# Kernel optimization log

Hardware: AMD Instinct MI355X
Metric: run time of the kernel (lower is better)

Reference implementation:

```python
import jax, jax.numpy as jnp
import numpy as np

D = 1024

def setup_inputs() -> dict:
    key = jax.random.key(0)
    kx, kw = jax.random.split(key)
    x = jax.random.normal(kx, (4, 2048, D), dtype=jnp.float32)
    # nn.Linear(d, 3d, bias=False): weight [3d, d]; y = x @ W.T
    W = jax.random.normal(kw, (3 * D, D), dtype=jnp.float32) * (1.0 / np.sqrt(D))
    return {"x": x, "W": W}

def reference(x, W):
    d = x.shape[-1]
    qkv = jnp.einsum('bsd,ed->bse', x, W)  # [B,S,3d]
    q, k, v = jnp.split(qkv, 3, axis=2)
    att = jnp.einsum('bqd,bkd->bqk', q, k) * (1.0 / jnp.sqrt(jnp.asarray(d, x.dtype)))
    att = jax.nn.softmax(att, axis=-1)
    y = jnp.einsum('bqk,bkd->bqd', att, v)
    return y
```

## Files before the change

### kernel.cpp

```cpp
#include <hip/hip_runtime.h>
#include <hip/hip_bf16.h>

typedef __attribute__((ext_vector_type(8))) short short8;
typedef __attribute__((ext_vector_type(4))) float f32x4;

typedef unsigned short u16;

__device__ __forceinline__ u16 f32_to_bf16(float f) {
    unsigned int u = __float_as_uint(f);
    u += 0x7fffu + ((u >> 16) & 1u);
    return (u16)(u >> 16);
}

__device__ __forceinline__ void gload16(const u16* g, u16* lds_base) {
    __builtin_amdgcn_global_load_lds(
        (const __attribute__((address_space(1))) void*)g,
        (__attribute__((address_space(3))) void*)lds_base, 16, 0, 0);
}

__device__ __forceinline__ void bar() { __builtin_amdgcn_s_barrier(); }
__device__ __forceinline__ void bar_end() {
    __builtin_amdgcn_sched_barrier(0);
    __builtin_amdgcn_s_barrier();
}
__device__ __forceinline__ void wait_vm8() {
    asm volatile("s_waitcnt vmcnt(8)" ::: "memory");
}
__device__ __forceinline__ void wait_vm7() {
    asm volatile("s_waitcnt vmcnt(7)" ::: "memory");
}
__device__ __forceinline__ void wait_vm6() {
    asm volatile("s_waitcnt vmcnt(6)" ::: "memory");
}
__device__ __forceinline__ void wait_vm0() {
    asm volatile("s_waitcnt vmcnt(0)" ::: "memory");
}

__global__ void cast_inputs(const float* __restrict__ x, u16* __restrict__ Xb,
                            const float* __restrict__ W, u16* __restrict__ Wb,
                            float* __restrict__ l,
                            int nx4, int nw4, int nl) {
    int i = blockIdx.x * blockDim.x + threadIdx.x;
    if (i >= nx4 + nw4) {
        int idx = i - (nx4 + nw4);
        if (idx < nl) l[idx] = 0.f;
        return;
    }
    const float* in; u16* out; int idx;
    if (i < nx4) { in = x; out = Xb; idx = i; }
    else { idx = i - nx4; in = W; out = Wb; }
    float4 v = ((const float4*)in)[idx];
    ushort4 o;
    o.x = f32_to_bf16(v.x); o.y = f32_to_bf16(v.y);
    o.z = f32_to_bf16(v.z); o.w = f32_to_bf16(v.w);
    ((ushort4*)out)[idx] = o;
}


struct Acc256 { f32x4 acc[8][4]; };
struct Acc192 { f32x4 acc[8][3]; };
struct Acc128 { f32x4 acc[8][2]; };

template<int MH>
__device__ __forceinline__ void rd_a(const u16* __restrict__ sA, int wr, int lane,
                                     int lr, short8 (&af)[4][2]) {
#pragma unroll
    for (int a2 = 0; a2 < 4; ++a2) {
        const int row = wr * 128 + MH * 64 + a2 * 16 + lr;
#pragma unroll
        for (int k2 = 0; k2 < 2; ++k2) {
            const int cb = (lane >> 4) + k2 * 4;
            af[a2][k2] = *(const short8*)(sA + row * 64 + ((cb ^ (lr & 7)) * 8));
        }
    }
}

template<int NH>
__device__ __forceinline__ void rd_b(const u16* __restrict__ sB, int wc, int lane,
                                     int lr, short8 (&bf)[2][2]) {
#pragma unroll
    for (int b2 = 0; b2 < 2; ++b2) {
        const int row = wc * 64 + NH * 32 + b2 * 16 + lr;
#pragma unroll
        for (int k2 = 0; k2 < 2; ++k2) {
            const int cb = (lane >> 4) + k2 * 4;
            bf[b2][k2] = *(const short8*)(sB + row * 64 + ((cb ^ (lr & 7)) * 8));
        }
    }
}

template<int MH, int NH>
__device__ __forceinline__ void mm_q(Acc256& fr, const short8 (&af)[4][2],
                                     const short8 (&bf)[2][2]) {
    __builtin_amdgcn_s_setprio(1);
#pragma unroll
    for (int a2 = 0; a2 < 4; ++a2)
#pragma unroll
        for (int b2 = 0; b2 < 2; ++b2)
#pragma unroll
            for (int k2 = 0; k2 < 2; ++k2)
                fr.acc[MH * 4 + a2][NH * 2 + b2] =
                    __builtin_amdgcn_mfma_f32_16x16x32_bf16(
                        af[a2][k2], bf[b2][k2],
                        fr.acc[MH * 4 + a2][NH * 2 + b2], 0, 0, 0);
    __builtin_amdgcn_s_setprio(0);
}

__device__ __forceinline__ void rd_b01(const u16* __restrict__ sB, int wc, int lane,
                                       int lr, short8 (&bf)[2][2]) {
#pragma unroll
    for (int b2 = 0; b2 < 2; ++b2) {
        const int row = wc * 48 + b2 * 16 + lr;
#pragma unroll
        for (int k2 = 0; k2 < 2; ++k2) {
            const int cb = (lane >> 4) + k2 * 4;
            bf[b2][k2] = *(const short8*)(sB + row * 64 + ((cb ^ (lr & 7)) * 8));
        }
    }
}

__device__ __forceinline__ void rd_b2(const u16* __restrict__ sB, int wc, int lane,
                                      int lr, short8 (&bf)[2]) {
    const int row = wc * 48 + 32 + lr;
#pragma unroll
    for (int k2 = 0; k2 < 2; ++k2) {
        const int cb = (lane >> 4) + k2 * 4;
        bf[k2] = *(const short8*)(sB + row * 64 + ((cb ^ (lr & 7)) * 8));
    }
}

template<int MH>
__device__ __forceinline__ void mm_b01(Acc192& fr, const short8 (&af)[4][2],
                                       const short8 (&bf)[2][2]) {
    __builtin_amdgcn_s_setprio(1);
#pragma unroll
    for (int a2 = 0; a2 < 4; ++a2)
#pragma unroll
        for (int b2 = 0; b2 < 2; ++b2)
#pragma unroll
            for (int k2 = 0; k2 < 2; ++k2)
                fr.acc[MH * 4 + a2][b2] =
                    __builtin_amdgcn_mfma_f32_16x16x32_bf16(
                        af[a2][k2], bf[b2][k2],
                        fr.acc[MH * 4 + a2][b2], 0, 0, 0);
    __builtin_amdgcn_s_setprio(0);
}

template<int MH>
__device__ __forceinline__ void mm_b2(Acc192& fr, const short8 (&af)[4][2],
                                      const short8 (&bf)[2]) {
    __builtin_amdgcn_s_setprio(1);
#pragma unroll
    for (int a2 = 0; a2 < 4; ++a2)
#pragma unroll
        for (int k2 = 0; k2 < 2; ++k2)
            fr.acc[MH * 4 + a2][2] =
                __builtin_amdgcn_mfma_f32_16x16x32_bf16(
                    af[a2][k2], bf[k2], fr.acc[MH * 4 + a2][2], 0, 0, 0);
    __builtin_amdgcn_s_setprio(0);
}

__device__ __forceinline__ void rd_bb(const u16* __restrict__ sB, int wc, int lane,
                                      int lr, short8 (&bf)[2][2]) {
#pragma unroll
    for (int b2 = 0; b2 < 2; ++b2) {
        const int row = wc * 32 + b2 * 16 + lr;
#pragma unroll
        for (int k2 = 0; k2 < 2; ++k2) {
            const int cb = (lane >> 4) + k2 * 4;
            bf[b2][k2] = *(const short8*)(sB + row * 64 + ((cb ^ (lr & 7)) * 8));
        }
    }
}

template<int MH>
__device__ __forceinline__ void mm_n128(Acc128& fr, const short8 (&af)[4][2],
                                        const short8 (&bf)[2][2]) {
    __builtin_amdgcn_s_setprio(1);
#pragma unroll
    for (int a2 = 0; a2 < 4; ++a2)
#pragma unroll
        for (int b2 = 0; b2 < 2; ++b2)
#pragma unroll
            for (int k2 = 0; k2 < 2; ++k2)
                fr.acc[MH * 4 + a2][b2] =
                    __builtin_amdgcn_mfma_f32_16x16x32_bf16(
                        af[a2][k2], bf[b2][k2],
                        fr.acc[MH * 4 + a2][b2], 0, 0, 0);
    __builtin_amdgcn_s_setprio(0);
}

__device__ __forceinline__ void gemm_core_256(
    const u16* __restrict__ A, const u16* __restrict__ Bt,
    int K, int lda, int ldb, int row0, int col0, u16* sm, Acc256& fr)
{
    const int t    = threadIdx.x;
    const int lane = t & 63;
    const int wave = t >> 6;
    const int wr   = wave >> 2;
    const int wc   = wave & 3;
    const int lr   = lane & 15;
    const int srow = lane >> 3;
    const int gc   = (lane & 7) ^ srow;

    const u16* const sA0 = sm;
    const u16* const sA1 = sm + 16384;
    const u16* const sB0 = sm + 32768;
    const u16* const sB1 = sm + 49152;

#pragma unroll
    for (int a = 0; a < 8; ++a)
#pragma unroll
        for (int b = 0; b < 4; ++b)
            fr.acc[a][b] = (f32x4){0.f, 0.f, 0.f, 0.f};

    const u16* aB = A  + (long long)(row0 + wave * 8 + srow) * lda + gc * 8;
    const u16* bB = Bt + (long long)(col0 + wave * 8 + srow) * ldb + gc * 8;
    u16* const sAw = sm + wave * 512;
    u16* const sBw = sm + 32768 + wave * 512;

    auto stageA = [&](int kt) {
        u16* d = sAw + (kt & 1) * 16384;
        const u16* g = aB + kt * 64;
#pragma unroll
        for (int r4 = 0; r4 < 4; ++r4)
            gload16(g + (long long)(r4 * 64) * lda, d + r4 * 4096);
    };
    auto stageB = [&](int kt) {
        u16* d = sBw + (kt & 1) * 16384;
        const u16* g = bB + kt * 64;
#pragma unroll
        for (int r4 = 0; r4 < 4; ++r4)
            gload16(g + (long long)(r4 * 64) * ldb, d + r4 * 4096);
    };

    stageA(0); stageB(0); stageA(1); stageB(1);
    wait_vm8();
    bar();

    const int NI = K >> 7;
    short8 af[4][2], bfa[2][2], bfb[2][2];
#pragma unroll 1
    for (int i = 0; i < NI; ++i) {
        const bool more = (i + 1 < NI);
        const int t2 = 2 * i + 2;

        rd_a<0>(sA0, wr, lane, lr, af);
        rd_b<0>(sB0, wc, lane, lr, bfa);
        bar();
        mm_q<0, 0>(fr, af, bfa);
        bar_end();

        rd_b<1>(sB0, wc, lane, lr, bfb);
        bar();
        mm_q<0, 1>(fr, af, bfb);
        bar_end();

        rd_a<1>(sA0, wr, lane, lr, af);
        if (more) stageB(t2);
        bar();
        mm_q<1, 1>(fr, af, bfb);
        bar_end();

        if (more) stageA(t2);
        bar();
        mm_q<1, 0>(fr, af, bfa);
        if (more) wait_vm8(); else wait_vm0();
        bar_end();

        rd_a<0>(sA1, wr, lane, lr, af);
        rd_b<0>(sB1, wc, lane, lr, bfa);
        bar();
        mm_q<0, 0>(fr, af, bfa);
        bar_end();

        rd_b<1>(sB1, wc, lane, lr, bfb);
        bar();
        mm_q<0, 1>(fr, af, bfb);
        bar_end();

        rd_a<1>(sA1, wr, lane, lr, af);
        if (more) stageB(t2 + 1);
        bar();
        mm_q<1, 1>(fr, af, bfb);
        bar_end();

        if (more) stageA(t2 + 1);
        bar();
        mm_q<1, 0>(fr, af, bfa);
        if (more) wait_vm8();
        bar_end();
    }
}

__device__ __forceinline__ void gemm_core_192(
    const u16* __restrict__ A, const u16* __restrict__ Bt,
    int K, int lda, int ldb, int row0, int col0, u16* sm, Acc192& fr)
{
    const int t    = threadIdx.x;
    const int lane = t & 63;
    const int wave = t >> 6;
    const int wr   = wave >> 2;
    const int wc   = wave & 3;
    const int lr   = lane & 15;
    const int srow = lane >> 3;
    const int gc   = (lane & 7) ^ srow;

    const u16* const sA0 = sm;
    const u16* const sA1 = sm + 16384;
    const u16* const sB0 = sm + 32768;
    const u16* const sB1 = sm + 45056;

#pragma unroll
    for (int a = 0; a < 8; ++a)
#pragma unroll
        for (int b = 0; b < 3; ++b)
            fr.acc[a][b] = (f32x4){0.f, 0.f, 0.f, 0.f};

    const u16* aB = A  + (long long)(row0 + wave * 8 + srow) * lda + gc * 8;
    const u16* bB = Bt + (long long)(col0 + wave * 8 + srow) * ldb + gc * 8;
    u16* const sAw = sm + wave * 512;
    u16* const sBw = sm + 32768 + wave * 512;

    auto stageA = [&](int kt) {
        u16* d = sAw + (kt & 1) * 16384;
        const u16* g = aB + kt * 64;
#pragma unroll
        for (int r4 = 0; r4 < 4; ++r4)
            gload16(g + (long long)(r4 * 64) * lda, d + r4 * 4096);
    };
    auto stageB = [&](int kt) {
        u16* d = sBw + (kt & 1) * 12288;
        const u16* g = bB + kt * 64;
#pragma unroll
        for (int r4 = 0; r4 < 3; ++r4)
            gload16(g + (long long)(r4 * 64) * ldb, d + r4 * 4096);
    };

    stageA(0); stageB(0); stageA(1); stageB(1);
    wait_vm7();
    bar();

    const int NI = K >> 7;
    short8 af[4][2], bfa[2][2], bfb[2];
#pragma unroll 1
    for (int i = 0; i < NI; ++i) {
        const bool more = (i + 1 < NI);
        const int t2 = 2 * i + 2;

        rd_a<0>(sA0, wr, lane, lr, af);
        rd_b01(sB0, wc, lane, lr, bfa);
        bar();
        mm_b01<0>(fr, af, bfa);
        bar_end();

        rd_b2(sB0, wc, lane, lr, bfb);
        bar();
        mm_b2<0>(fr, af, bfb);
        bar_end();

        rd_a<1>(sA0, wr, lane, lr, af);
        if (more) stageB(t2);
        bar();
        mm_b2<1>(fr, af, bfb);
        bar_end();

        if (more) stageA(t2);
        bar();
        mm_b01<1>(fr, af, bfa);
        if (more) wait_vm7(); else wait_vm0();
        bar_end();

        rd_a<0>(sA1, wr, lane, lr, af);
        rd_b01(sB1, wc, lane, lr, bfa);
        bar();
        mm_b01<0>(fr, af, bfa);
        bar_end();

        rd_b2(sB1, wc, lane, lr, bfb);
        bar();
        mm_b2<0>(fr, af, bfb);
        bar_end();

        rd_a<1>(sA1, wr, lane, lr, af);
        if (more) stageB(t2 + 1);
        bar();
        mm_b2<1>(fr, af, bfb);
        bar_end();

        if (more) stageA(t2 + 1);
        bar();
        mm_b01<1>(fr, af, bfa);
        if (more) wait_vm7();
        bar_end();
    }
}

__device__ __forceinline__ void gemm_core_n128(
    const u16* __restrict__ A, const u16* __restrict__ Bt,
    int K, int lda, int ldb, int row0, int col0, u16* sm, Acc128& fr)
{
    const int t    = threadIdx.x;
    const int lane = t & 63;
    const int wave = t >> 6;
    const int wr   = wave >> 2;
    const int wc   = wave & 3;
    const int lr   = lane & 15;
    const int srow = lane >> 3;
    const int gc   = (lane & 7) ^ srow;

    const u16* const sA0 = sm;
    const u16* const sA1 = sm + 16384;
    const u16* const sB0 = sm + 32768;
    const u16* const sB1 = sm + 40960;

#pragma unroll
    for (int a = 0; a < 8; ++a)
#pragma unroll
        for (int b = 0; b < 2; ++b)
            fr.acc[a][b] = (f32x4){0.f, 0.f, 0.f, 0.f};

    const u16* aB = A  + (long long)(row0 + wave * 8 + srow) * lda + gc * 8;
    const u16* bB = Bt + (long long)(col0 + wave * 8 + srow) * ldb + gc * 8;
    u16* const sAw = sm + wave * 512;
    u16* const sBw = sm + 32768 + wave * 512;

    auto stageA = [&](int kt) {
        u16* d = sAw + (kt & 1) * 16384;
        const u16* g = aB + kt * 64;
#pragma unroll
        for (int r4 = 0; r4 < 4; ++r4)
            gload16(g + (long long)(r4 * 64) * lda, d + r4 * 4096);
    };
    auto stageB = [&](int kt) {
        u16* d = sBw + (kt & 1) * 8192;
        const u16* g = bB + kt * 64;
#pragma unroll
        for (int r4 = 0; r4 < 2; ++r4)
            gload16(g + (long long)(r4 * 64) * ldb, d + r4 * 4096);
    };

    stageB(0); stageA(0); stageB(1); stageA(1);
    wait_vm6();
    bar();

    const int NI = K >> 7;
    short8 af[4][2], bf[2][2];
#pragma unroll 1
    for (int i = 0; i < NI; ++i) {
        const bool more = (i + 1 < NI);
        const int t2 = 2 * i + 2;

        rd_a<0>(sA0, wr, lane, lr, af);
        rd_bb(sB0, wc, lane, lr, bf);
        if (more) stageB(t2);
        bar();
        mm_n128<0>(fr, af, bf);
        bar_end();

        rd_a<1>(sA0, wr, lane, lr, af);
        if (more) stageA(t2);
        bar();
        mm_n128<1>(fr, af, bf);
        if (more) wait_vm6(); else wait_vm0();
        bar_end();

        rd_a<0>(sA1, wr, lane, lr, af);
        rd_bb(sB1, wc, lane, lr, bf);
        if (more) stageB(t2 + 1);
        bar();
        mm_n128<0>(fr, af, bf);
        bar_end();

        rd_a<1>(sA1, wr, lane, lr, af);
        if (more) stageA(t2 + 1);
        bar();
        mm_n128<1>(fr, af, bf);
        if (more) wait_vm6();
        bar_end();
    }
}


__global__ __launch_bounds__(512, 1) void gemm_qkv(
    const u16* __restrict__ Xb, const u16* __restrict__ Wb,
    u16* __restrict__ QK, u16* __restrict__ VT)
{
    __shared__ u16 sm[57344];
    const int row0 = blockIdx.y * 256;
    const int col0 = blockIdx.x * 192;

    Acc192 fr;
    gemm_core_192(Xb, Wb, 1024, 1024, 1024, row0, col0, sm, fr);

    const int lane = threadIdx.x & 63;
    const int wave = threadIdx.x >> 6;
    const int wr = wave >> 2, wc = wave & 3;
    const int cr = (lane >> 4) * 4, cc = lane & 15;

#pragma unroll
    for (int a = 0; a < 8; ++a) {
        const int grow = row0 + wr * 128 + a * 16 + cr;
#pragma unroll
        for (int b = 0; b < 3; ++b) {
            const int gcol = col0 + wc * 48 + b * 16 + cc;
            if (gcol < 2048) {
#pragma unroll
                for (int r = 0; r < 4; ++r)
                    QK[(long long)(grow + r) * 2048 + gcol] =
                        f32_to_bf16(fr.acc[a][b][r]);
            } else {
                const int bz = grow >> 11, s = grow & 2047;
                const int d = gcol - 2048;
                ushort4 o;
                o.x = f32_to_bf16(fr.acc[a][b][0]);
                o.y = f32_to_bf16(fr.acc[a][b][1]);
                o.z = f32_to_bf16(fr.acc[a][b][2]);
                o.w = f32_to_bf16(fr.acc[a][b][3]);
                *(ushort4*)(&VT[((long long)(bz * 1024 + d)) * 2048 + s]) = o;
            }
        }
    }
}

__global__ __launch_bounds__(512, 1) void gemm_s_exp(
    const u16* __restrict__ QK, u16* __restrict__ E, float* __restrict__ l)
{
    __shared__ u16 sm[65536];
    const long long boff = (long long)blockIdx.z * 2048 * 2048;
    const u16* Q  = QK + boff;
    const u16* Kp = QK + boff + 1024;
    u16* Eb = E + boff;
    float* lb = l + (long long)blockIdx.z * 2048;
    const int row0 = blockIdx.y * 256;
    const int col0 = blockIdx.x * 256;

    Acc256 fr;
    gemm_core_256(Q, Kp, 1024, 2048, 2048, row0, col0, sm, fr);

    const int lane = threadIdx.x & 63;
    const int wave = threadIdx.x >> 6;
    const int wr = wave >> 2, wc = wave & 3;
    const int cr = (lane >> 4) * 4, cc = lane & 15;

#pragma unroll
    for (int a = 0; a < 8; ++a) {
        float rs[4] = {0.f, 0.f, 0.f, 0.f};
#pragma unroll
        for (int b = 0; b < 4; ++b)
#pragma unroll
            for (int r = 0; r < 4; ++r) {
                float e = __expf(fr.acc[a][b][r] * 0.03125f);
                rs[r] += e;
                int grow = row0 + wr * 128 + a * 16 + cr + r;
                int gcol = col0 + wc * 64 + b * 16 + cc;
                Eb[(long long)grow * 2048 + gcol] = f32_to_bf16(e);
            }
#pragma unroll
        for (int r = 0; r < 4; ++r) {
#pragma unroll
            for (int m = 1; m < 16; m <<= 1) rs[r] += __shfl_xor(rs[r], m, 64);
            if ((lane & 15) == 0)
                atomicAdd(&lb[row0 + wr * 128 + a * 16 + cr + r], rs[r]);
        }
    }
}

__global__ __launch_bounds__(512, 1) void gemm_pv(
    const u16* __restrict__ E, const u16* __restrict__ VT,
    const float* __restrict__ l, float* __restrict__ Y)
{
    __shared__ u16 sm[49152];
    const u16* Eb  = E  + (long long)blockIdx.z * 2048 * 2048;
    const u16* VTb = VT + (long long)blockIdx.z * 1024 * 2048;
    const float* lb = l + (long long)blockIdx.z * 2048;
    float* Yb = Y + (long long)blockIdx.z * 2048 * 1024;
    const int row0 = blockIdx.x * 256;
    const int col0 = blockIdx.y * 128;

    Acc128 fr;
    gemm_core_n128(Eb, VTb, 2048, 2048, 2048, row0, col0, sm, fr);

    const int lane = threadIdx.x & 63;
    const int wave = threadIdx.x >> 6;
    const int wr = wave >> 2, wc = wave & 3;
    const int cr = (lane >> 4) * 4, cc = lane & 15;

#pragma unroll
    for (int a = 0; a < 8; ++a) {
        const int q0 = row0 + wr * 128 + a * 16 + cr;
        const float4 l4 = *(const float4*)(&lb[q0]);
        const float inv0 = 1.0f / l4.x, inv1 = 1.0f / l4.y;
        const float inv2 = 1.0f / l4.z, inv3 = 1.0f / l4.w;
#pragma unroll
        for (int b = 0; b < 2; ++b) {
            const int d = col0 + wc * 32 + b * 16 + cc;
            Yb[(long long)(q0 + 0) * 1024 + d] = fr.acc[a][b][0] * inv0;
            Yb[(long long)(q0 + 1) * 1024 + d] = fr.acc[a][b][1] * inv1;
            Yb[(long long)(q0 + 2) * 1024 + d] = fr.acc[a][b][2] * inv2;
            Yb[(long long)(q0 + 3) * 1024 + d] = fr.acc[a][b][3] * inv3;
        }
    }
}

extern "C" void kernel_launch(void* const* d_in, const int* in_sizes, int n_in,
                              void* d_out, int out_size, void* d_ws, size_t ws_size,
                              hipStream_t stream) {
    const float* x = (const float*)d_in[0];
    const float* W = (const float*)d_in[1];
    float* out = (float*)d_out;

    char* ws = (char*)d_ws;
    u16*   Xb = (u16*)(ws);
    u16*   Wb = (u16*)(ws + 16777216LL);
    u16*   QK = (u16*)(ws + 23068672LL);
    u16*   VT = (u16*)(ws + 56623104LL);
    u16*   E  = (u16*)(ws + 73400320LL);
    float* l  = (float*)(ws + 106954752LL);

    const int nx4 = 8192 * 1024 / 4, nw4 = 3072 * 1024 / 4;
    cast_inputs<<<11296, 256, 0, stream>>>(x, Xb, W, Wb, l, nx4, nw4, 8192);
    gemm_qkv<<<dim3(16, 32, 1), 512, 0, stream>>>(Xb, Wb, QK, VT);
    gemm_s_exp<<<dim3(8, 8, 4), 512, 0, stream>>>(QK, E, l);
    gemm_pv<<<dim3(8, 8, 4), 512, 0, stream>>>(E, VT, l, out);
}
```

Baseline: 222.9 us.

## Software-pipeline LDS fragment reads with MFMA using double-buffered registers

Restructures the GEMM main loop so the LDS-to-register fragment reads for the next sub-step are issued alongside the MFMAs of the current sub-step, using ping-pong register sets (afP/afQ, bfaP/bfaQ). This removes the separate read-then-barrier-then-compute phases and their paired barriers. The global stage waits change to vmcnt(3) to match the new issue order. The extra register sets raise VGPR pressure and could reduce occupancy or cause spills, and the hand-placed barrier and waitcnt ordering has to stay correct to avoid races.

```diff
diff --git a/kernel.cpp b/kernel.cpp
--- a/kernel.cpp
+++ b/kernel.cpp
@@ -31,6 +31,9 @@
 }
 __device__ __forceinline__ void wait_vm6() {
     asm volatile("s_waitcnt vmcnt(6)" ::: "memory");
+}
+__device__ __forceinline__ void wait_vm3() {
+    asm volatile("s_waitcnt vmcnt(3)" ::: "memory");
 }
 __device__ __forceinline__ void wait_vm0() {
     asm volatile("s_waitcnt vmcnt(0)" ::: "memory");
@@ -341,58 +344,56 @@
     wait_vm7();
     bar();
 
-    const int NI = K >> 7;
-    short8 af[4][2], bfa[2][2], bfb[2];
+    short8 afP[4][2], afQ[4][2], bfaP[2][2], bfaQ[2][2], bfb[2];
+    rd_a<0>(sA0, wr, lane, lr, afP);
+    rd_b01(sB0, wc, lane, lr, bfaP);
+
+    const int NT = K >> 6;
 #pragma unroll 1
-    for (int i = 0; i < NI; ++i) {
-        const bool more = (i + 1 < NI);
-        const int t2 = 2 * i + 2;
-
-        rd_a<0>(sA0, wr, lane, lr, af);
-        rd_b01(sB0, wc, lane, lr, bfa);
-        bar();
-        mm_b01<0>(fr, af, bfa);
-        bar_end();
+    for (int i = 0; i < NT; i += 2) {
+        const bool more = (i + 2 < NT);
 
         rd_b2(sB0, wc, lane, lr, bfb);
-        bar();
-        mm_b2<0>(fr, af, bfb);
-        bar_end();
-
-        rd_a<1>(sA0, wr, lane, lr, af);
-        if (more) stageB(t2);
-        bar();
-        mm_b2<1>(fr, af, bfb);
-        bar_end();
-
-        if (more) stageA(t2);
-        bar();
-        mm_b01<1>(fr, af, bfa);
-        if (more) wait_vm7(); else wait_vm0();
-        bar_end();
-
-        rd_a<0>(sA1, wr, lane, lr, af);
-        rd_b01(sB1, wc, lane, lr, bfa);
-        bar();
-        mm_b01<0>(fr, af, bfa);
-        bar_end();
+        mm_b01<0>(fr, afP, bfaP);
+        bar();
+
+        rd_a<1>(sA0, wr, lane, lr, afQ);
+        mm_b2<0>(fr, afP, bfb);
+        bar();
+
+        mm_b2<1>(fr, afQ, bfb);
+        __builtin_amdgcn_sched_barrier(0);
+        if (more) { stageB(i + 2); wait_vm3(); } else wait_vm0();
+        bar();
+
+        rd_a<0>(sA1, wr, lane, lr, afP);
+        rd_b01(sB1, wc, lane, lr, bfaQ);
+        mm_b01<1>(fr, afQ, bfaP);
+        __builtin_amdgcn_sched_barrier(0);
+        if (more) stageA(i + 2);
+        bar();
 
         rd_b2(sB1, wc, lane, lr, bfb);
-        bar();
-        mm_b2<0>(fr, af, bfb);
-        bar_end();
-
-        rd_a<1>(sA1, wr, lane, lr, af);
-        if (more) stageB(t2 + 1);
-        bar();
-        mm_b2<1>(fr, af, bfb);
-        bar_end();
-
-        if (more) stageA(t2 + 1);
-        bar();
-        mm_b01<1>(fr, af, bfa);
-        if (more) wait_vm7();
-        bar_end();
+        mm_b01<0>(fr, afP, bfaQ);
+        bar();
+
+        rd_a<1>(sA1, wr, lane, lr, afQ);
+        mm_b2<0>(fr, afP, bfb);
+        bar();
+
+        mm_b2<1>(fr, afQ, bfb);
+        __builtin_amdgcn_sched_barrier(0);
+        if (more) { stageB(i + 3); wait_vm3(); } else wait_vm0();
+        bar();
+
+        if (more) {
+            rd_a<0>(sA0, wr, lane, lr, afP);
+            rd_b01(sB0, wc, lane, lr, bfaP);
+        }
+        mm_b01<1>(fr, afQ, bfaQ);
+        __builtin_amdgcn_sched_barrier(0);
+        if (more) stageA(i + 3);
+        bar();
     }
 }
 
```

After: 226.0 us. No clear change (+1.4%).
